# Kernel optimization log

Hardware: AMD Instinct MI355X
Metric: run time of the kernel (lower is better)

The kernel has to match this reference:

```python
import jax, jax.numpy as jnp
import numpy as np

EPS = 1e-6

def rms_norm(x, scale):
    # T5-style LayerNorm: RMS over last axis in fp32, then scale
    x32 = x.astype(jnp.float32)
    mean2 = jnp.mean(jnp.square(x32), axis=-1, keepdims=True)
    return (x32 * jax.lax.rsqrt(mean2 + EPS)) * scale

def setup_inputs() -> dict:
    key = jax.random.key(0)
    ks = jax.random.split(key, 7)
    B, S, E, H, D = 2, 2048, 2048, 16, 128
    w_std = 1.0 / np.sqrt(E)
    x = jax.random.normal(ks[0], (B, S, E), jnp.float32)
    wq = jax.random.normal(ks[1], (E, H, D), jnp.float32) * w_std
    wk = jax.random.normal(ks[2], (E, H, D), jnp.float32) * w_std
    wv = jax.random.normal(ks[3], (E, H, D), jnp.float32) * w_std
    wo = jax.random.normal(ks[4], (H, D, E), jnp.float32) * (1.0 / np.sqrt(H * D))
    q_scale = jnp.ones((D,), jnp.float32)
    k_scale = jnp.ones((D,), jnp.float32)
    return {"x": x, "wq": wq, "wk": wk, "wv": wv, "wo": wo,
            "q_scale": q_scale, "k_scale": k_scale}

def reference(x, wq, wk, wv, wo, q_scale, k_scale):
    # Q/K/V projections: [B,S,E] x [E,H,D] -> [B,S,H,D]
    q = jnp.einsum('bse,ehd->bshd', x, wq)
    k = jnp.einsum('bse,ehd->bshd', x, wk)
    v = jnp.einsum('bse,ehd->bshd', x, wv)
    # QK layernorm (RMS, no scaling by 1/sqrt(d) in this variant)
    qn = rms_norm(q, q_scale)
    kn = rms_norm(k, k_scale)
    # Naive attention: explicit [B,H,Q,K] scores
    scores = jnp.einsum('bqhd,bkhd->bhqk', qn, kn)
    attn = jax.nn.softmax(scores, axis=-1)
    out = jnp.einsum('bhqk,bkhd->bqhd', attn, v)
    # Output projection: [B,S,H,D] x [H,D,E] -> [B,S,E]
    return jnp.einsum('bqhd,hde->bqe', out, wo)
```

## Files before the change

kernel.cpp:

```cpp
#include <hip/hip_runtime.h>
#include <hip/hip_bf16.h>
#include <math.h>

#define BATCH 2
#define SEQ   2048
#define EMB   2048
#define NH    16
#define HD    128

typedef __attribute__((ext_vector_type(8))) short short8;
typedef __attribute__((ext_vector_type(8))) _Float16 half8;
typedef __attribute__((ext_vector_type(4))) float floatx4;

__device__ inline void async_load16(const void* g, void* l) {
    __builtin_amdgcn_global_load_lds(
        (const __attribute__((address_space(1))) unsigned int*)g,
        (__attribute__((address_space(3))) unsigned int*)l, 16, 0, 0);
}

__device__ inline unsigned short bf16_bits(float f) {
    __hip_bfloat16 b = __float2bfloat16(f);
    return *(unsigned short*)&b;
}
__device__ inline unsigned short fp16_bits(float f) {
    _Float16 h = (_Float16)f;
    return *(unsigned short*)&h;
}

#define GT 128
#define GK 32

__global__ __launch_bounds__(256) void gemm_bf16(
    const unsigned short* __restrict__ A,
    const unsigned short* __restrict__ Bt,
    float* __restrict__ C, int M, int N, int K)
{
    __shared__ unsigned short As[GT * GK];
    __shared__ unsigned short Bs[GT * GK];

    const int tid  = threadIdx.x;
    const int w    = tid >> 6;
    const int lane = tid & 63;
    const int wr   = w >> 1, wc = w & 1;
    const int row0 = blockIdx.y * GT;
    const int col0 = blockIdx.x * GT;

    floatx4 acc[4][4];
    #pragma unroll
    for (int i = 0; i < 4; i++)
        #pragma unroll
        for (int j = 0; j < 4; j++)
            acc[i][j] = (floatx4){0.f, 0.f, 0.f, 0.f};

    const int srow  = lane >> 2;
    const int skoff = (lane & 3) * 8;
    const int fm = lane & 15;
    const int fk = (lane >> 4) * 8;

    for (int k0 = 0; k0 < K; k0 += GK) {
        #pragma unroll
        for (int t = 0; t < 2; t++) {
            const int c = w * 2 + t;
            async_load16(A  + (size_t)(row0 + c * 16 + srow) * K + k0 + skoff, (char*)As + c * 1024);
            async_load16(Bt + (size_t)(col0 + c * 16 + srow) * K + k0 + skoff, (char*)Bs + c * 1024);
        }
        __syncthreads();

        short8 af[4], bf[4];
        #pragma unroll
        for (int i = 0; i < 4; i++) {
            af[i] = *(const short8*)&As[(wr * 64 + i * 16 + fm) * GK + fk];
            bf[i] = *(const short8*)&Bs[(wc * 64 + i * 16 + fm) * GK + fk];
        }
        #pragma unroll
        for (int i = 0; i < 4; i++)
            #pragma unroll
            for (int j = 0; j < 4; j++)
                acc[i][j] = __builtin_amdgcn_mfma_f32_16x16x32_bf16(af[i], bf[j], acc[i][j], 0, 0, 0);
        __syncthreads();
    }

    const int quad = lane >> 4;
    #pragma unroll
    for (int i = 0; i < 4; i++)
        #pragma unroll
        for (int j = 0; j < 4; j++) {
            const size_t base = (size_t)(row0 + wr * 64 + i * 16 + quad * 4) * N
                              + col0 + wc * 64 + j * 16 + fm;
            #pragma unroll
            for (int r = 0; r < 4; r++)
                C[base + (size_t)r * N] = acc[i][j][r];
        }
}

__global__ __launch_bounds__(256) void gemm_v_vt(
    const unsigned short* __restrict__ A,
    const unsigned short* __restrict__ Bt,
    unsigned short* __restrict__ Vt, int K)
{
    __shared__ char smem[2 * 128 * 72 * 2] __attribute__((aligned(16)));
    unsigned short* As = (unsigned short*)smem;
    unsigned short* Bs = (unsigned short*)(smem + 8192);
    typedef unsigned short stage_row[72];
    stage_row* stage0 = (stage_row*)smem;

    const int tid  = threadIdx.x;
    const int w    = tid >> 6;
    const int lane = tid & 63;
    const int wr   = w >> 1, wc = w & 1;
    const int row0 = blockIdx.y * GT;
    const int col0 = blockIdx.x * GT;

    floatx4 acc[4][4];
    #pragma unroll
    for (int i = 0; i < 4; i++)
        #pragma unroll
        for (int j = 0; j < 4; j++)
            acc[i][j] = (floatx4){0.f, 0.f, 0.f, 0.f};

    const int srow  = lane >> 2;
    const int skoff = (lane & 3) * 8;
    const int fm = lane & 15;
    const int fk = (lane >> 4) * 8;

    for (int k0 = 0; k0 < K; k0 += GK) {
        #pragma unroll
        for (int t = 0; t < 2; t++) {
            const int c = w * 2 + t;
            async_load16(A  + (size_t)(row0 + c * 16 + srow) * K + k0 + skoff, (char*)As + c * 1024);
            async_load16(Bt + (size_t)(col0 + c * 16 + srow) * K + k0 + skoff, (char*)Bs + c * 1024);
        }
        __syncthreads();

        half8 af[4], bf[4];
        #pragma unroll
        for (int i = 0; i < 4; i++) {
            af[i] = *(const half8*)&As[(wr * 64 + i * 16 + fm) * GK + fk];
            bf[i] = *(const half8*)&Bs[(wc * 64 + i * 16 + fm) * GK + fk];
        }
        #pragma unroll
        for (int i = 0; i < 4; i++)
            #pragma unroll
            for (int j = 0; j < 4; j++)
                acc[i][j] = __builtin_amdgcn_mfma_f32_16x16x32_f16(af[i], bf[j], acc[i][j], 0, 0, 0);
        __syncthreads();
    }

    const int quad = lane >> 4;
    const int b  = row0 >> 11;
    const int h  = col0 >> 7;
    const int bh = b * NH + h;
    const int kt_base = (row0 & 2047) >> 6;

    #pragma unroll
    for (int i = 0; i < 4; i++)
        #pragma unroll
        for (int r = 0; r < 4; r++) {
            const int key = i * 16 + quad * 4 + r;
            #pragma unroll
            for (int j = 0; j < 4; j++) {
                const int d = wc * 64 + j * 16 + fm;
                stage0[wr * 128 + d][key] = fp16_bits(acc[i][j][r]);
            }
        }
    __syncthreads();

    const int d = tid >> 1, half = tid & 1;
    #pragma unroll
    for (int kt = 0; kt < 2; kt++) {
        const size_t ob = ((size_t)(bh * 32 + kt_base + kt)) * 8192 + (size_t)d * 64;
        #pragma unroll
        for (int cc = 0; cc < 4; cc++) {
            const int cs = half * 4 + cc;
            const int kb = (cs ^ (d & 7)) << 3;
            *(short8*)&Vt[ob + cs * 8] = *(const short8*)&stage0[kt * 128 + d][kb];
        }
    }
}

__global__ __launch_bounds__(256) void gemm_qk_rms(
    const unsigned short* __restrict__ A,
    const unsigned short* __restrict__ Bq, const unsigned short* __restrict__ Bk,
    const float* __restrict__ q_scale, const float* __restrict__ k_scale,
    unsigned short* __restrict__ Qf, unsigned short* __restrict__ Kf,
    int K)
{
    __shared__ unsigned short As[GT * GK];
    __shared__ unsigned short Bs[GT * GK];
    __shared__ float ws2[2][GT];

    const int z = blockIdx.z;
    const unsigned short* __restrict__ Bt = z ? Bk : Bq;
    const float* __restrict__ scale = z ? k_scale : q_scale;
    unsigned short* __restrict__ o = z ? Kf : Qf;
    const int swz = z;

    const int tid  = threadIdx.x;
    const int w    = tid >> 6;
    const int lane = tid & 63;
    const int wr   = w >> 1, wc = w & 1;
    const int row0 = blockIdx.y * GT;
    const int col0 = blockIdx.x * GT;

    floatx4 acc[4][4];
    #pragma unroll
    for (int i = 0; i < 4; i++)
        #pragma unroll
        for (int j = 0; j < 4; j++)
            acc[i][j] = (floatx4){0.f, 0.f, 0.f, 0.f};

    const int srow  = lane >> 2;
    const int skoff = (lane & 3) * 8;
    const int fm = lane & 15;
    const int fk = (lane >> 4) * 8;

    for (int k0 = 0; k0 < K; k0 += GK) {
        #pragma unroll
        for (int t = 0; t < 2; t++) {
            const int c = w * 2 + t;
            async_load16(A  + (size_t)(row0 + c * 16 + srow) * K + k0 + skoff, (char*)As + c * 1024);
            async_load16(Bt + (size_t)(col0 + c * 16 + srow) * K + k0 + skoff, (char*)Bs + c * 1024);
        }
        __syncthreads();

        half8 af[4], bf[4];
        #pragma unroll
        for (int i = 0; i < 4; i++) {
            af[i] = *(const half8*)&As[(wr * 64 + i * 16 + fm) * GK + fk];
            bf[i] = *(const half8*)&Bs[(wc * 64 + i * 16 + fm) * GK + fk];
        }
        #pragma unroll
        for (int i = 0; i < 4; i++)
            #pragma unroll
            for (int j = 0; j < 4; j++)
                acc[i][j] = __builtin_amdgcn_mfma_f32_16x16x32_f16(af[i], bf[j], acc[i][j], 0, 0, 0);
        __syncthreads();
    }

    const int quad = lane >> 4;

    float sq[4][4];
    #pragma unroll
    for (int i = 0; i < 4; i++)
        #pragma unroll
        for (int r = 0; r < 4; r++) {
            float s2 = 0.f;
            #pragma unroll
            for (int j = 0; j < 4; j++) s2 += acc[i][j][r] * acc[i][j][r];
            s2 += __shfl_xor(s2, 1);
            s2 += __shfl_xor(s2, 2);
            s2 += __shfl_xor(s2, 4);
            s2 += __shfl_xor(s2, 8);
            sq[i][r] = s2;
        }
    if (fm == 0) {
        #pragma unroll
        for (int i = 0; i < 4; i++)
            #pragma unroll
            for (int r = 0; r < 4; r++)
                ws2[wc][wr * 64 + i * 16 + quad * 4 + r] = sq[i][r];
    }
    __syncthreads();

    const int hh = col0 >> 7;
    float scv[4];
    #pragma unroll
    for (int j = 0; j < 4; j++) scv[j] = scale[wc * 64 + j * 16 + fm];

    #pragma unroll
    for (int i = 0; i < 4; i++)
        #pragma unroll
        for (int r = 0; r < 4; r++) {
            const int lrow = wr * 64 + i * 16 + quad * 4 + r;
            const int row  = row0 + lrow;
            const int bb = row >> 11, s = row & 2047;
            const float inv = rsqrtf((ws2[0][lrow] + ws2[1][lrow]) * (1.0f / HD) + 1e-6f);
            const size_t ob = ((size_t)(bb * NH + hh) * SEQ + s) * 128;
            #pragma unroll
            for (int j = 0; j < 4; j++) {
                const int d = wc * 64 + j * 16 + fm;
                const float val = acc[i][j][r] * inv * scv[j];
                const int dd = swz ? ((((d >> 3) ^ (s & 15)) << 3) | (d & 7)) : d;
                o[ob + dd] = fp16_bits(val);
            }
        }
}

__global__ __launch_bounds__(256) void cast_f16(
    const float* __restrict__ in, unsigned short* __restrict__ o, int n)
{
    int i = (blockIdx.x * 256 + threadIdx.x) * 4;
    if (i >= n) return;
    float4 v = *(const float4*)&in[i];
    ushort4 h;
    h.x = fp16_bits(v.x);
    h.y = fp16_bits(v.y);
    h.z = fp16_bits(v.z);
    h.w = fp16_bits(v.w);
    *(ushort4*)&o[i] = h;
}

__global__ __launch_bounds__(256) void prep_weights(
    const float* __restrict__ wq, const float* __restrict__ wk,
    const float* __restrict__ wv, const float* __restrict__ wo,
    unsigned short* __restrict__ wqF, unsigned short* __restrict__ wkF,
    unsigned short* __restrict__ wvF, unsigned short* __restrict__ woT)
{
    __shared__ float tile[32][33];
    const int z = blockIdx.z;
    const float* __restrict__ W = (z == 0) ? wq : (z == 1) ? wk : (z == 2) ? wv : wo;
    const int k0 = blockIdx.y * 32, n0 = blockIdx.x * 32;
    const int tx = threadIdx.x, ty = threadIdx.y;
    #pragma unroll
    for (int i = 0; i < 4; i++)
        tile[ty + i * 8][tx] = W[(size_t)(k0 + ty + i * 8) * 2048 + n0 + tx];
    __syncthreads();
    if (z < 3) {
        unsigned short* __restrict__ t = (z == 0) ? wqF : (z == 1) ? wkF : wvF;
        #pragma unroll
        for (int i = 0; i < 4; i++)
            t[(size_t)(n0 + ty + i * 8) * 2048 + k0 + tx] = fp16_bits(tile[tx][ty + i * 8]);
    } else {
        #pragma unroll
        for (int i = 0; i < 4; i++)
            woT[(size_t)(n0 + ty + i * 8) * 2048 + k0 + tx] = bf16_bits(tile[tx][ty + i * 8]);
    }
}

#define ATQ 256
#define ATK 64

__global__ __launch_bounds__(512, 1) void attn14(
    const unsigned short* __restrict__ Qf, const unsigned short* __restrict__ Kf,
    const unsigned short* __restrict__ Vt, __hip_bfloat16* __restrict__ AO)
{
    __shared__ unsigned short Ks[2][ATK * 128];
    __shared__ unsigned short Vts[2][HD * 64];
    __shared__ unsigned short Ps[ATQ * 64];

    const int tid  = threadIdx.x;
    const int w    = tid >> 6;
    const int lane = tid & 63;
    const int quad = lane >> 4;
    const int fm   = lane & 15;
    const int bh = blockIdx.y;
    const int b = bh >> 4, h = bh & 15;
    const int q0 = blockIdx.x * ATQ;

    const size_t hbase = (size_t)(b * NH + h) * SEQ;

    half8 qf[2][4];
    #pragma unroll
    for (int i = 0; i < 2; i++) {
        const size_t row = hbase + q0 + w * 32 + i * 16 + fm;
        #pragma unroll
        for (int kc = 0; kc < 4; kc++)
            qf[i][kc] = *(const half8*)&Qf[row * 128 + kc * 32 + quad * 8];
    }

    floatx4 oacc[2][8];
    #pragma unroll
    for (int i = 0; i < 2; i++)
        #pragma unroll
        for (int df = 0; df < 8; df++)
            oacc[i][df] = (floatx4){0.f, 0.f, 0.f, 0.f};
    float m_[2][4], l_[2][4];
    #pragma unroll
    for (int i = 0; i < 2; i++)
        #pragma unroll
        for (int r = 0; r < 4; r++) { m_[i][r] = -1e30f; l_[i][r] = 0.f; }

    const unsigned short* gk0  = Kf + hbase * 128;
    const unsigned short* gvt0 = Vt + (size_t)bh * 32 * 8192;

    const int ch0 = w * 4;

    #pragma unroll
    for (int c = 0; c < 4; c++) {
        const int ch = ch0 + c;
        const size_t go = (size_t)(ch & 15) * 512 + lane * 8;
        if (ch < 16) async_load16(gk0  + go, (char*)Ks[0]  + ch * 1024);
        else         async_load16(gvt0 + go, (char*)Vts[0] + (ch - 16) * 1024);
    }
    __syncthreads();

    for (int ktile = 0; ktile < SEQ / ATK; ktile++) {
        const int cur = ktile & 1;

        if (ktile + 1 < SEQ / ATK) {
            const unsigned short* gk  = gk0  + (size_t)(ktile + 1) * ATK * 128;
            const unsigned short* gvt = gvt0 + (size_t)(ktile + 1) * 8192;
            #pragma unroll
            for (int c = 0; c < 4; c++) {
                const int ch = ch0 + c;
                const size_t go = (size_t)(ch & 15) * 512 + lane * 8;
                if (ch < 16) async_load16(gk  + go, (char*)Ks[1 - cur]  + ch * 1024);
                else         async_load16(gvt + go, (char*)Vts[1 - cur] + (ch - 16) * 1024);
            }
        }

        floatx4 sacc[2][4];
        #pragma unroll
        for (int i = 0; i < 2; i++)
            #pragma unroll
            for (int jf = 0; jf < 4; jf++)
                sacc[i][jf] = (floatx4){0.f, 0.f, 0.f, 0.f};
        #pragma unroll
        for (int kc = 0; kc < 4; kc++)
            #pragma unroll
            for (int jf = 0; jf < 4; jf++) {
                const int koff = (jf * 16 + fm) * 128 + (((kc * 4 + quad) ^ fm) << 3);
                half8 k8 = *(const half8*)&Ks[cur][koff];
                #pragma unroll
                for (int i = 0; i < 2; i++)
                    sacc[i][jf] = __builtin_amdgcn_mfma_f32_16x16x32_f16(qf[i][kc], k8, sacc[i][jf], 0, 0, 0);
            }

        float alpha_[2][4];
        #pragma unroll
        for (int i = 0; i < 2; i++)
            #pragma unroll
            for (int r = 0; r < 4; r++) {
                float mx = fmaxf(fmaxf(sacc[i][0][r], sacc[i][1][r]),
                                 fmaxf(sacc[i][2][r], sacc[i][3][r]));
                mx = fmaxf(mx, __shfl_xor(mx, 1));
                mx = fmaxf(mx, __shfl_xor(mx, 2));
                mx = fmaxf(mx, __shfl_xor(mx, 4));
                mx = fmaxf(mx, __shfl_xor(mx, 8));
                const float mold = m_[i][r];
                const float mnew = fmaxf(mold, mx);
                const float al = __expf(mold - mnew);
                m_[i][r] = mnew;
                alpha_[i][r] = al;
                float rs = 0.f;
                #pragma unroll
                for (int jf = 0; jf < 4; jf++) {
                    float p = __expf(sacc[i][jf][r] - mnew);
                    sacc[i][jf][r] = p;
                    rs += p;
                }
                rs += __shfl_xor(rs, 1);
                rs += __shfl_xor(rs, 2);
                rs += __shfl_xor(rs, 4);
                rs += __shfl_xor(rs, 8);
                l_[i][r] = l_[i][r] * al + rs;
            }
        #pragma unroll
        for (int i = 0; i < 2; i++)
            #pragma unroll
            for (int df = 0; df < 8; df++)
                #pragma unroll
                for (int r = 0; r < 4; r++)
                    oacc[i][df][r] *= alpha_[i][r];

        #pragma unroll
        for (int i = 0; i < 2; i++)
            #pragma unroll
            for (int jf = 0; jf < 4; jf++)
                #pragma unroll
                for (int r = 0; r < 4; r++) {
                    const int row = w * 32 + i * 16 + quad * 4 + r;
                    const int chunk = jf * 2 + (fm >> 3);
                    const int colp = ((chunk ^ (row & 7)) << 3) | (fm & 7);
                    Ps[row * 64 + colp] = fp16_bits(sacc[i][jf][r]);
                }

        #pragma unroll
        for (int kc2 = 0; kc2 < 2; kc2++) {
            half8 ap[2];
            #pragma unroll
            for (int i = 0; i < 2; i++) {
                const int row = w * 32 + i * 16 + fm;
                ap[i] = *(const half8*)&Ps[row * 64 + (((kc2 * 4 + quad) ^ (row & 7)) << 3)];
            }
            #pragma unroll
            for (int df = 0; df < 8; df++) {
                const int d = df * 16 + fm;
                half8 bv = *(const half8*)&Vts[cur][d * 64 + (((kc2 * 4 + quad) ^ (d & 7)) << 3)];
                #pragma unroll
                for (int i = 0; i < 2; i++)
                    oacc[i][df] = __builtin_amdgcn_mfma_f32_16x16x32_f16(ap[i], bv, oacc[i][df], 0, 0, 0);
            }
        }

        __syncthreads();
    }

    const size_t obase = ((size_t)b * SEQ * NH + h) * HD;
    const size_t rstr = (size_t)NH * HD;
    float linv[2][4];
    #pragma unroll
    for (int i = 0; i < 2; i++)
        #pragma unroll
        for (int r = 0; r < 4; r++) linv[i][r] = 1.0f / l_[i][r];
    #pragma unroll
    for (int i = 0; i < 2; i++)
        #pragma unroll
        for (int df = 0; df < 8; df++)
            #pragma unroll
            for (int r = 0; r < 4; r++) {
                const int row = q0 + w * 32 + i * 16 + quad * 4 + r;
                const int d = df * 16 + fm;
                AO[obase + (size_t)row * rstr + d] = __float2bfloat16(oacc[i][df][r] * linv[i][r]);
            }
}

extern "C" void kernel_launch(void* const* d_in, const int* in_sizes, int n_in,
                              void* d_out, int out_size, void* d_ws, size_t ws_size,
                              hipStream_t stream) {
    const float* x  = (const float*)d_in[0];
    const float* wq = (const float*)d_in[1];
    const float* wk = (const float*)d_in[2];
    const float* wv = (const float*)d_in[3];
    const float* wo = (const float*)d_in[4];
    const float* q_scale = (const float*)d_in[5];
    const float* k_scale = (const float*)d_in[6];
    float* out = (float*)d_out;

    const size_t T = (size_t)BATCH * SEQ * NH * HD;
    const size_t W = (size_t)EMB * NH * HD;

    unsigned short* xf   = (unsigned short*)d_ws;
    unsigned short* aob  = xf + T;
    unsigned short* Qf   = aob + T;
    unsigned short* Kf   = Qf + T;
    unsigned short* Vtb  = Kf + T;
    unsigned short* wqF  = Vtb + T;
    unsigned short* wkF  = wqF + W;
    unsigned short* wvF  = wkF + W;
    unsigned short* woT  = wvF + W;

    const int M = BATCH * SEQ;
    const int N = NH * HD;
    const int K = EMB;

    cast_f16<<<(int)(T / 4 + 255) / 256, 256, 0, stream>>>(x, xf, (int)T);
    prep_weights<<<dim3(64, 64, 4), dim3(32, 8), 0, stream>>>(
        wq, wk, wv, wo, wqF, wkF, wvF, woT);

    gemm_qk_rms<<<dim3(N / GT, M / GT, 2), 256, 0, stream>>>(
        xf, wqF, wkF, q_scale, k_scale, Qf, Kf, K);
    gemm_v_vt<<<dim3(N / GT, M / GT), 256, 0, stream>>>(xf, wvF, Vtb, K);

    attn14<<<dim3(SEQ / ATQ, BATCH * NH), 512, 0, stream>>>(Qf, Kf, Vtb, (__hip_bfloat16*)aob);

    gemm_bf16<<<dim3(EMB / GT, M / GT), 256, 0, stream>>>(aob, woT, out, M, EMB, NH * HD);
}
```

Measured before the change: 505.9 us.

## Fuse Q and K projections into one block sharing the A tile, merge prep kernels

Q and K projections now run in one 512-thread block that loads the shared x tile once and computes both Q and K outputs with separate wave halves. This halves the x-tile traffic for these two GEMMs. Blocks are remapped with an XCD-aware swizzle to improve L2 locality. The x cast is folded into the weight-prep kernel to save a launch. The trade-off is larger blocks with more LDS, which may reduce occupancy.

```diff
diff --git a/kernel.cpp b/kernel.cpp
--- a/kernel.cpp
+++ b/kernel.cpp
@@ -90,6 +90,123 @@
             #pragma unroll
             for (int r = 0; r < 4; r++)
                 C[base + (size_t)r * N] = acc[i][j][r];
+        }
+}
+
+__global__ __launch_bounds__(512) void gemm_qk_fused(
+    const unsigned short* __restrict__ A,
+    const unsigned short* __restrict__ Bq, const unsigned short* __restrict__ Bk,
+    const float* __restrict__ q_scale, const float* __restrict__ k_scale,
+    unsigned short* __restrict__ Qf, unsigned short* __restrict__ Kf, int K)
+{
+    __shared__ unsigned short As[GT * GK];
+    __shared__ unsigned short BsQ[GT * GK];
+    __shared__ unsigned short BsK[GT * GK];
+    __shared__ float ws2[2][2][GT];
+
+    const int tid  = threadIdx.x;
+    const int w    = tid >> 6;
+    const int lane = tid & 63;
+    const int half = w >> 2;
+    const int wq   = w & 3;
+    const int wr   = wq >> 1, wc = wq & 1;
+
+    const int L   = blockIdx.x;
+    const int xcd = L & 7;
+    const int idx = L >> 3;
+    const int bx  = (xcd & 1) * 8 + (idx & 7);
+    const int by  = (xcd >> 1) * 8 + (idx >> 3);
+    const int row0 = by * GT;
+    const int col0 = bx * GT;
+
+    floatx4 acc[4][4];
+    #pragma unroll
+    for (int i = 0; i < 4; i++)
+        #pragma unroll
+        for (int j = 0; j < 4; j++)
+            acc[i][j] = (floatx4){0.f, 0.f, 0.f, 0.f};
+
+    const int srow  = lane >> 2;
+    const int skoff = (lane & 3) * 8;
+    const int fm = lane & 15;
+    const int fk = (lane >> 4) * 8;
+
+    for (int k0 = 0; k0 < K; k0 += GK) {
+        #pragma unroll
+        for (int c = 0; c < 3; c++) {
+            const int ch  = w * 3 + c;
+            const int sub = ch & 7;
+            const int base = (ch < 8) ? row0 : col0;
+            const size_t off = (size_t)(base + sub * 16 + srow) * K + k0 + skoff;
+            if (ch < 8)       async_load16(A  + off, (char*)As  + sub * 1024);
+            else if (ch < 16) async_load16(Bq + off, (char*)BsQ + sub * 1024);
+            else              async_load16(Bk + off, (char*)BsK + sub * 1024);
+        }
+        __syncthreads();
+
+        const unsigned short* __restrict__ Bs = half ? BsK : BsQ;
+        half8 af[4], bf[4];
+        #pragma unroll
+        for (int i = 0; i < 4; i++) {
+            af[i] = *(const half8*)&As[(wr * 64 + i * 16 + fm) * GK + fk];
+            bf[i] = *(const half8*)&Bs[(wc * 64 + i * 16 + fm) * GK + fk];
+        }
+        #pragma unroll
+        for (int i = 0; i < 4; i++)
+            #pragma unroll
+            for (int j = 0; j < 4; j++)
+                acc[i][j] = __builtin_amdgcn_mfma_f32_16x16x32_f16(af[i], bf[j], acc[i][j], 0, 0, 0);
+        __syncthreads();
+    }
+
+    const int quad = lane >> 4;
+    const float* __restrict__ scale = half ? k_scale : q_scale;
+    unsigned short* __restrict__ o = half ? Kf : Qf;
+    const int hh = col0 >> 7;
+
+    float sq[4][4];
+    #pragma unroll
+    for (int i = 0; i < 4; i++)
+        #pragma unroll
+        for (int r = 0; r < 4; r++) {
+            float s2 = 0.f;
+            #pragma unroll
+            for (int j = 0; j < 4; j++) s2 += acc[i][j][r] * acc[i][j][r];
+            s2 += __shfl_xor(s2, 1);
+            s2 += __shfl_xor(s2, 2);
+            s2 += __shfl_xor(s2, 4);
+            s2 += __shfl_xor(s2, 8);
+            sq[i][r] = s2;
+        }
+    if (fm == 0) {
+        #pragma unroll
+        for (int i = 0; i < 4; i++)
+            #pragma unroll
+            for (int r = 0; r < 4; r++)
+                ws2[half][wc][wr * 64 + i * 16 + quad * 4 + r] = sq[i][r];
+    }
+    __syncthreads();
+
+    float scv[4];
+    #pragma unroll
+    for (int j = 0; j < 4; j++) scv[j] = scale[wc * 64 + j * 16 + fm];
+
+    #pragma unroll
+    for (int i = 0; i < 4; i++)
+        #pragma unroll
+        for (int r = 0; r < 4; r++) {
+            const int lrow = wr * 64 + i * 16 + quad * 4 + r;
+            const int row  = row0 + lrow;
+            const int bb = row >> 11, s = row & 2047;
+            const float inv = rsqrtf((ws2[half][0][lrow] + ws2[half][1][lrow]) * (1.0f / HD) + 1e-6f);
+            const size_t ob = ((size_t)(bb * NH + hh) * SEQ + s) * 128;
+            #pragma unroll
+            for (int j = 0; j < 4; j++) {
+                const int d = wc * 64 + j * 16 + fm;
+                const float val = acc[i][j][r] * inv * scv[j];
+                const int dd = half ? ((((d >> 3) ^ (s & 15)) << 3) | (d & 7)) : d;
+                o[ob + dd] = fp16_bits(val);
+            }
         }
 }
 
@@ -178,139 +295,33 @@
     }
 }
 
-__global__ __launch_bounds__(256) void gemm_qk_rms(
-    const unsigned short* __restrict__ A,
-    const unsigned short* __restrict__ Bq, const unsigned short* __restrict__ Bk,
-    const float* __restrict__ q_scale, const float* __restrict__ k_scale,
-    unsigned short* __restrict__ Qf, unsigned short* __restrict__ Kf,
-    int K)
-{
-    __shared__ unsigned short As[GT * GK];
-    __shared__ unsigned short Bs[GT * GK];
-    __shared__ float ws2[2][GT];
-
-    const int z = blockIdx.z;
-    const unsigned short* __restrict__ Bt = z ? Bk : Bq;
-    const float* __restrict__ scale = z ? k_scale : q_scale;
-    unsigned short* __restrict__ o = z ? Kf : Qf;
-    const int swz = z;
-
-    const int tid  = threadIdx.x;
-    const int w    = tid >> 6;
-    const int lane = tid & 63;
-    const int wr   = w >> 1, wc = w & 1;
-    const int row0 = blockIdx.y * GT;
-    const int col0 = blockIdx.x * GT;
-
-    floatx4 acc[4][4];
-    #pragma unroll
-    for (int i = 0; i < 4; i++)
-        #pragma unroll
-        for (int j = 0; j < 4; j++)
-            acc[i][j] = (floatx4){0.f, 0.f, 0.f, 0.f};
-
-    const int srow  = lane >> 2;
-    const int skoff = (lane & 3) * 8;
-    const int fm = lane & 15;
-    const int fk = (lane >> 4) * 8;
-
-    for (int k0 = 0; k0 < K; k0 += GK) {
-        #pragma unroll
-        for (int t = 0; t < 2; t++) {
-            const int c = w * 2 + t;
-            async_load16(A  + (size_t)(row0 + c * 16 + srow) * K + k0 + skoff, (char*)As + c * 1024);
-            async_load16(Bt + (size_t)(col0 + c * 16 + srow) * K + k0 + skoff, (char*)Bs + c * 1024);
-        }
-        __syncthreads();
-
-        half8 af[4], bf[4];
-        #pragma unroll
-        for (int i = 0; i < 4; i++) {
-            af[i] = *(const half8*)&As[(wr * 64 + i * 16 + fm) * GK + fk];
-            bf[i] = *(const half8*)&Bs[(wc * 64 + i * 16 + fm) * GK + fk];
-        }
-        #pragma unroll
-        for (int i = 0; i < 4; i++)
-            #pragma unroll
-            for (int j = 0; j < 4; j++)
-                acc[i][j] = __builtin_amdgcn_mfma_f32_16x16x32_f16(af[i], bf[j], acc[i][j], 0, 0, 0);
-        __syncthreads();
-    }
-
-    const int quad = lane >> 4;
-
-    float sq[4][4];
-    #pragma unroll
-    for (int i = 0; i < 4; i++)
-        #pragma unroll
-        for (int r = 0; r < 4; r++) {
-            float s2 = 0.f;
-            #pragma unroll
-            for (int j = 0; j < 4; j++) s2 += acc[i][j][r] * acc[i][j][r];
-            s2 += __shfl_xor(s2, 1);
-            s2 += __shfl_xor(s2, 2);
-            s2 += __shfl_xor(s2, 4);
-            s2 += __shfl_xor(s2, 8);
-            sq[i][r] = s2;
-        }
-    if (fm == 0) {
-        #pragma unroll
-        for (int i = 0; i < 4; i++)
-            #pragma unroll
-            for (int r = 0; r < 4; r++)
-                ws2[wc][wr * 64 + i * 16 + quad * 4 + r] = sq[i][r];
-    }
-    __syncthreads();
-
-    const int hh = col0 >> 7;
-    float scv[4];
-    #pragma unroll
-    for (int j = 0; j < 4; j++) scv[j] = scale[wc * 64 + j * 16 + fm];
-
-    #pragma unroll
-    for (int i = 0; i < 4; i++)
-        #pragma unroll
-        for (int r = 0; r < 4; r++) {
-            const int lrow = wr * 64 + i * 16 + quad * 4 + r;
-            const int row  = row0 + lrow;
-            const int bb = row >> 11, s = row & 2047;
-            const float inv = rsqrtf((ws2[0][lrow] + ws2[1][lrow]) * (1.0f / HD) + 1e-6f);
-            const size_t ob = ((size_t)(bb * NH + hh) * SEQ + s) * 128;
-            #pragma unroll
-            for (int j = 0; j < 4; j++) {
-                const int d = wc * 64 + j * 16 + fm;
-                const float val = acc[i][j][r] * inv * scv[j];
-                const int dd = swz ? ((((d >> 3) ^ (s & 15)) << 3) | (d & 7)) : d;
-                o[ob + dd] = fp16_bits(val);
-            }
-        }
-}
-
-__global__ __launch_bounds__(256) void cast_f16(
-    const float* __restrict__ in, unsigned short* __restrict__ o, int n)
-{
-    int i = (blockIdx.x * 256 + threadIdx.x) * 4;
-    if (i >= n) return;
-    float4 v = *(const float4*)&in[i];
-    ushort4 h;
-    h.x = fp16_bits(v.x);
-    h.y = fp16_bits(v.y);
-    h.z = fp16_bits(v.z);
-    h.w = fp16_bits(v.w);
-    *(ushort4*)&o[i] = h;
-}
-
-__global__ __launch_bounds__(256) void prep_weights(
+__global__ __launch_bounds__(256) void prep_all(
     const float* __restrict__ wq, const float* __restrict__ wk,
     const float* __restrict__ wv, const float* __restrict__ wo,
+    const float* __restrict__ x,
     unsigned short* __restrict__ wqF, unsigned short* __restrict__ wkF,
-    unsigned short* __restrict__ wvF, unsigned short* __restrict__ woT)
+    unsigned short* __restrict__ wvF, unsigned short* __restrict__ woT,
+    unsigned short* __restrict__ xf)
 {
     __shared__ float tile[32][33];
     const int z = blockIdx.z;
+    const int tx = threadIdx.x, ty = threadIdx.y;
+
+    if (z == 4) {
+        const int blk = blockIdx.y * 64 + blockIdx.x;
+        const size_t base = (size_t)blk * 2048 + (ty * 32 + tx) * 8;
+        float4 a = *(const float4*)&x[base];
+        float4 b = *(const float4*)&x[base + 4];
+        ushort4 ha, hb;
+        ha.x = fp16_bits(a.x); ha.y = fp16_bits(a.y); ha.z = fp16_bits(a.z); ha.w = fp16_bits(a.w);
+        hb.x = fp16_bits(b.x); hb.y = fp16_bits(b.y); hb.z = fp16_bits(b.z); hb.w = fp16_bits(b.w);
+        *(ushort4*)&xf[base] = ha;
+        *(ushort4*)&xf[base + 4] = hb;
+        return;
+    }
+
     const float* __restrict__ W = (z == 0) ? wq : (z == 1) ? wk : (z == 2) ? wv : wo;
     const int k0 = blockIdx.y * 32, n0 = blockIdx.x * 32;
-    const int tx = threadIdx.x, ty = threadIdx.y;
     #pragma unroll
     for (int i = 0; i < 4; i++)
         tile[ty + i * 8][tx] = W[(size_t)(k0 + ty + i * 8) * 2048 + n0 + tx];
@@ -534,11 +545,10 @@
     const int N = NH * HD;
     const int K = EMB;
 
-    cast_f16<<<(int)(T / 4 + 255) / 256, 256, 0, stream>>>(x, xf, (int)T);
-    prep_weights<<<dim3(64, 64, 4), dim3(32, 8), 0, stream>>>(
-        wq, wk, wv, wo, wqF, wkF, wvF, woT);
-
-    gemm_qk_rms<<<dim3(N / GT, M / GT, 2), 256, 0, stream>>>(
+    prep_all<<<dim3(64, 64, 5), dim3(32, 8), 0, stream>>>(
+        wq, wk, wv, wo, x, wqF, wkF, wvF, woT, xf);
+
+    gemm_qk_fused<<<512, 512, 0, stream>>>(
         xf, wqF, wkF, q_scale, k_scale, Qf, Kf, K);
     gemm_v_vt<<<dim3(N / GT, M / GT), 256, 0, stream>>>(xf, wvF, Vtb, K);
 
```

Measured after the change: 467.4 us. 1.08x faster.
